# Kernel optimization log

Measured on AMD Instinct MI355X. Metric: run time of the kernel, lower is better.

The kernel has to match this reference:

```python
import jax, jax.numpy as jnp
import numpy as np

B, T, N, C, H, E = 1, 10, 10000, 4, 128, 160000


def setup_inputs() -> dict:
    key = jax.random.key(0)
    ks = jax.random.split(key, 16)
    def g(k, shape, fan_in):
        return jax.random.normal(k, shape, jnp.float32) / np.sqrt(fan_in).astype(np.float32)
    return {
        "inputs": jax.random.normal(ks[0], (B, T, N, C), jnp.float32),
        "msg_fc1_w": g(ks[1], (3, 2 * H, H), 2 * H),
        "msg_fc1_b": jnp.zeros((3, H), jnp.float32),
        "msg_fc2_w": g(ks[2], (3, H, H), H),
        "msg_fc2_b": jnp.zeros((3, H), jnp.float32),
        "hidden_r_w": g(ks[3], (H, H), H),
        "hidden_i_w": g(ks[4], (H, H), H),
        "hidden_h_w": g(ks[5], (H, H), H),
        "input_r_w": g(ks[6], (C, H), C),
        "input_r_b": jnp.zeros((H,), jnp.float32),
        "input_i_w": g(ks[7], (C, H), C),
        "input_i_b": jnp.zeros((H,), jnp.float32),
        "input_n_w": g(ks[8], (C, H), C),
        "input_n_b": jnp.zeros((H,), jnp.float32),
        "out1_w": g(ks[9], (H, H), H),
        "out1_b": jnp.zeros((H,), jnp.float32),
        "out2_w": g(ks[10], (H, H), H),
        "out2_b": jnp.zeros((H,), jnp.float32),
        "out3_w": g(ks[11], (H, C), H),
        "out3_b": jnp.zeros((C,), jnp.float32),
        "edge_index": jax.random.randint(ks[12], (2, E), 0, N, jnp.int32),
        "burn_in_steps": T,
    }


def reference(inputs, msg_fc1_w, msg_fc1_b, msg_fc2_w, msg_fc2_b,
              hidden_r_w, hidden_i_w, hidden_h_w,
              input_r_w, input_r_b, input_i_w, input_i_b, input_n_w, input_n_b,
              out1_w, out1_b, out2_w, out2_b, out3_w, out3_b,
              edge_index, burn_in_steps):
    row, col = edge_index[0], edge_index[1]
    Bv, Tv, Nv, Cv = inputs.shape
    Hv = hidden_r_w.shape[0]

    def single_step(x, hidden):
        # gather edge endpoint states: [B,E,2H]
        pre = jnp.concatenate([hidden[:, row, :], hidden[:, col, :]], axis=-1)
        # 3 msg branches vectorized over k (dropout p=0 / eval mode)
        m = jnp.tanh(jnp.einsum('bef,kfh->kbeh', pre, msg_fc1_w) + msg_fc1_b[:, None, None, :])
        m = jnp.tanh(jnp.einsum('kbeh,khd->kbed', m, msg_fc2_w) + msg_fc2_b[:, None, None, :])
        all_msgs = m.sum(0)  # [B,E,H]
        # scatter-add into receiver nodes (col)
        agg = jnp.zeros((Bv, Nv, Hv), x.dtype).at[:, col, :].add(all_msgs)
        r = jax.nn.sigmoid(x @ input_r_w + input_r_b + agg @ hidden_r_w)
        i = jax.nn.sigmoid(x @ input_i_w + input_i_b + agg @ hidden_i_w)
        n = jnp.tanh(x @ input_n_w + input_n_b + r * (agg @ hidden_h_w))
        hidden = (1 - i) * n + i * hidden
        p = jax.nn.relu(hidden @ out1_w + out1_b)
        p = jax.nn.relu(p @ out2_w + out2_b)
        p = jax.nn.relu(p @ out3_w + out3_b)
        return x + p, hidden

    def step(carry, xs):
        hidden, prev_pred = carry
        x_t, t = xs
        use_input = jnp.logical_or(t < burn_in_steps, t == 0)
        ins = jnp.where(use_input, x_t, prev_pred)
        pred, hidden = single_step(ins, hidden)
        return (hidden, pred), pred

    hidden0 = jnp.zeros((Bv, Nv, Hv), inputs.dtype)
    xs = (jnp.moveaxis(inputs, 1, 0), jnp.arange(Tv))  # [T,B,N,C]
    _, preds = jax.lax.scan(step, (hidden0, inputs[:, 0]), xs)
    return jnp.moveaxis(preds, 0, 1)  # [B,T,N,C]
```

## Files before the change

### kernel.cpp

```cpp
#include <hip/hip_runtime.h>

#define TT 10
#define NN 10000
#define CC 4
#define HH 128
#define EE 160000

typedef unsigned char u8;
typedef unsigned short u16;
typedef unsigned int u32;
typedef __attribute__((ext_vector_type(8))) short bf16x8;
typedef __attribute__((ext_vector_type(4))) float f32x4;

#define FW2 0
#define FW1 192
#define FO  768
#define FG  896
#define NFRAG 1184

__device__ __forceinline__ u16 f2b(float x){
  union { float f; u32 u; } v; v.f = x;
  return (u16)((v.u + 0x7fffu + ((v.u >> 16) & 1u)) >> 16);
}
__device__ __forceinline__ float b2f(u16 b){
  union { u32 u; float f; } v; v.u = ((u32)b) << 16;
  return v.f;
}
__device__ __forceinline__ float fast_tanh(float x){
  float e = __builtin_amdgcn_exp2f(x * 2.885390081777927f);
  return 1.f - 2.f * __builtin_amdgcn_rcpf(e + 1.f);
}
__device__ __forceinline__ f32x4 zero4(){ f32x4 z = {0.f,0.f,0.f,0.f}; return z; }
__device__ __forceinline__ f32x4 mfmab(bf16x8 a, bf16x8 b, f32x4 c){
  return __builtin_amdgcn_mfma_f32_16x16x32_bf16(a, b, c, 0, 0, 0);
}
__device__ __forceinline__ bf16x8 ldA(const u16* L, int row, int sl){
  return *(const bf16x8*)(L + (row << 7) + ((sl ^ (row & 7)) << 3));
}
__device__ __forceinline__ bf16x8 ldB(const u16* packs, int frag, int lane){
  return *(const bf16x8*)(packs + frag*512 + lane*8);
}

struct PSrc { const float* w2; const float* w1; const float* o1; const float* o2;
              const float* gr; const float* gi; const float* gh; };

__global__ void pack_weights(PSrc ps, u16* __restrict__ dst){
  int f = blockIdx.x, l = threadIdx.x;
  const float* src; int comp, kt, ct;
  if (f < 192){
    comp = f / 96; int g = f % 96;
    int br = g >> 5, rem = g & 31; kt = rem >> 3; ct = rem & 7;
    src = ps.w2 + (size_t)br*HH*HH;
  } else if (f < 768){
    int g = f - 192; int m = g / 96; int rem = g % 96;
    comp = rem >> 5; int idx = rem & 31; kt = idx >> 3; ct = idx & 7;
    src = ps.w1 + (size_t)m*HH*HH;
  } else if (f < 896){
    int g = f - 768; int mat = g >> 6; int rem = g & 63;
    comp = rem >> 5; int idx = rem & 31; kt = idx >> 3; ct = idx & 7;
    src = mat ? ps.o2 : ps.o1;
  } else {
    int g = f - 896; int mat = g / 96; int rem = g % 96;
    comp = rem >> 5; int idx = rem & 31; kt = idx >> 3; ct = idx & 7;
    src = mat == 0 ? ps.gr : (mat == 1 ? ps.gi : ps.gh);
  }
  int col = (ct << 4) + (l & 15);
  u16* d = dst + f*512 + l*8;
  #pragma unroll
  for (int j = 0; j < 8; ++j){
    int kk = (kt << 5) + ((l >> 4) << 3) + j;
    float v = src[kk*HH + col];
    u16 c0 = f2b(v); float r = v - b2f(c0);
    u16 c1 = f2b(r); r -= b2f(c1);
    u16 c2 = f2b(r);
    d[j] = comp == 0 ? c0 : (comp == 1 ? c1 : c2);
  }
}

__global__ void hist_kernel(const int* __restrict__ edge, int* __restrict__ hist){
  int i = blockIdx.x*256 + threadIdx.x;
  if (i < EE) atomicAdd(&hist[edge[EE + i]], 1);
}
__global__ void scan_kernel(const int* __restrict__ hist, int* __restrict__ cursor){
  __shared__ int part[256];
  __shared__ int partx[256];
  int tid = threadIdx.x;
  int base = tid*40;
  int s = 0;
  for (int j = 0; j < 40; ++j){ int b = base+j; if (b < NN) s += hist[b]; }
  part[tid] = s;
  __syncthreads();
  if (tid == 0){ int acc = 0; for (int i = 0; i < 256; ++i){ partx[i] = acc; acc += part[i]; } }
  __syncthreads();
  int acc = partx[tid];
  for (int j = 0; j < 40; ++j){ int b = base+j; if (b < NN){ cursor[b] = acc; acc += hist[b]; } }
}
__global__ void scatter_kernel(const int* __restrict__ edge, int* __restrict__ cursor,
                               int* __restrict__ pr, int* __restrict__ pc){
  int i = blockIdx.x*256 + threadIdx.x;
  if (i < EE){
    int r = edge[i], c = edge[EE + i];
    int pos = atomicAdd(&cursor[c], 1);
    pr[pos] = r; pc[pos] = c;
  }
}

__global__ __launch_bounds__(256)
void uv_kernel(const float* __restrict__ hid, const u16* __restrict__ packs,
               float* __restrict__ UV){
  __shared__ __align__(16) u16 h0[32*128], h1[32*128], h2[32*128];
  const int tid = threadIdx.x;
  const int lane = tid & 63, wid = tid >> 6;
  const int n0 = blockIdx.x << 5;

  #pragma unroll
  for (int it = 0; it < 4; ++it){
    int s = tid + (it << 8);
    int r = s >> 5, c4 = s & 31;
    int node = n0 + r; if (node > NN-1) node = NN-1;
    float4 v = *(const float4*)(hid + (size_t)node*HH + (c4 << 2));
    ushort4 q0, q1, q2;
    const float* pv = (const float*)&v;
    u16* q0p = (u16*)&q0; u16* q1p = (u16*)&q1; u16* q2p = (u16*)&q2;
    #pragma unroll
    for (int e = 0; e < 4; ++e){
      float x = pv[e];
      u16 a0 = f2b(x); float rr = x - b2f(a0);
      u16 a1 = f2b(rr); rr -= b2f(a1);
      q0p[e] = a0; q1p[e] = a1; q2p[e] = f2b(rr);
    }
    int idx = (r << 7) + (((c4 >> 1) ^ (r & 7)) << 3) + ((c4 & 1) << 2);
    *(ushort4*)(h0 + idx) = q0;
    *(ushort4*)(h1 + idx) = q1;
    *(ushort4*)(h2 + idx) = q2;
  }
  __syncthreads();

  const int ct0 = wid << 1;
  const int r0 = lane & 15, r1 = r0 + 16, kg = lane >> 4;

  for (int m = 0; m < 6; ++m){
    f32x4 acc[2][2];
    acc[0][0]=zero4(); acc[0][1]=zero4(); acc[1][0]=zero4(); acc[1][1]=zero4();
    #pragma unroll
    for (int kt = 0; kt < 4; ++kt){
      int sl = (kt << 2) + kg;
      bf16x8 a00 = ldA(h0, r0, sl), a01 = ldA(h1, r0, sl), a02 = ldA(h2, r0, sl);
      bf16x8 a10 = ldA(h0, r1, sl), a11 = ldA(h1, r1, sl), a12 = ldA(h2, r1, sl);
      #pragma unroll
      for (int ctl = 0; ctl < 2; ++ctl){
        int fb = FW1 + m*96 + (kt << 3) + ct0 + ctl;
        bf16x8 b0 = ldB(packs, fb,      lane);
        bf16x8 b1 = ldB(packs, fb + 32, lane);
        bf16x8 b2 = ldB(packs, fb + 64, lane);
        acc[0][ctl] = mfmab(a00, b0, acc[0][ctl]);
        acc[0][ctl] = mfmab(a01, b0, acc[0][ctl]);
        acc[0][ctl] = mfmab(a00, b1, acc[0][ctl]);
        acc[0][ctl] = mfmab(a02, b0, acc[0][ctl]);
        acc[0][ctl] = mfmab(a01, b1, acc[0][ctl]);
        acc[0][ctl] = mfmab(a00, b2, acc[0][ctl]);
        acc[1][ctl] = mfmab(a10, b0, acc[1][ctl]);
        acc[1][ctl] = mfmab(a11, b0, acc[1][ctl]);
        acc[1][ctl] = mfmab(a10, b1, acc[1][ctl]);
        acc[1][ctl] = mfmab(a12, b0, acc[1][ctl]);
        acc[1][ctl] = mfmab(a11, b1, acc[1][ctl]);
        acc[1][ctl] = mfmab(a10, b2, acc[1][ctl]);
      }
    }
    #pragma unroll
    for (int ctl = 0; ctl < 2; ++ctl)
      #pragma unroll
      for (int rt = 0; rt < 2; ++rt)
        #pragma unroll
        for (int j = 0; j < 4; ++j){
          int row = (rt << 4) + (kg << 2) + j;
          int col = ((ct0 + ctl) << 4) + r0;
          int node = n0 + row;
          if (node < NN) UV[((size_t)m*NN + node)*HH + col] = acc[rt][ctl][j];
        }
  }
}

__global__ __launch_bounds__(256)
void edge_kernel(const int* __restrict__ pr, const int* __restrict__ pc,
                 const float* __restrict__ UV,
                 const float* __restrict__ b1, const float* __restrict__ b2,
                 const u16* __restrict__ packs, float* __restrict__ agg){
  __shared__ __align__(16) u16 m1hi[32*128];
  __shared__ __align__(16) u16 m1lo[32*128];
  __shared__ int er[32], ec[32];
  const int tid = threadIdx.x;
  const int lane = tid & 63, wid = tid >> 6;
  const int e0 = blockIdx.x << 5;

  if (tid < 32) er[tid] = pr[e0 + tid];
  else if (tid < 64) ec[tid - 32] = pc[e0 + tid - 32];

  const int c4 = tid & 31;
  const int cOff = c4 << 2;
  const int ct0 = wid << 1;
  const int r0 = lane & 15, r1 = r0 + 16, kg = lane >> 4;

  f32x4 acc[2][2];
  acc[0][0]=zero4(); acc[0][1]=zero4(); acc[1][0]=zero4(); acc[1][1]=zero4();

  for (int k = 0; k < 3; ++k){
    __syncthreads();
    {
      float4 b = *(const float4*)(b1 + k*HH + cOff);
      const float* __restrict__ Ub = UV + (size_t)(2*k)*NN*HH;
      const float* __restrict__ Vb = UV + (size_t)(2*k + 1)*NN*HH;
      #pragma unroll
      for (int it = 0; it < 4; ++it){
        int e = (tid >> 5) + (it << 3);
        float4 u = *(const float4*)(Ub + (size_t)er[e]*HH + cOff);
        float4 v = *(const float4*)(Vb + (size_t)ec[e]*HH + cOff);
        float m0 = fast_tanh(u.x + v.x + b.x);
        float m1 = fast_tanh(u.y + v.y + b.y);
        float m2 = fast_tanh(u.z + v.z + b.z);
        float m3 = fast_tanh(u.w + v.w + b.w);
        ushort4 hi, lo;
        hi.x = f2b(m0); lo.x = f2b(m0 - b2f(hi.x));
        hi.y = f2b(m1); lo.y = f2b(m1 - b2f(hi.y));
        hi.z = f2b(m2); lo.z = f2b(m2 - b2f(hi.z));
        hi.w = f2b(m3); lo.w = f2b(m3 - b2f(hi.w));
        int idx = (e << 7) + (((c4 >> 1) ^ (e & 7)) << 3) + ((c4 & 1) << 2);
        *(ushort4*)(m1hi + idx) = hi;
        *(ushort4*)(m1lo + idx) = lo;
      }
    }
    __syncthreads();

    f32x4 lacc[2][2];
    lacc[0][0]=zero4(); lacc[0][1]=zero4(); lacc[1][0]=zero4(); lacc[1][1]=zero4();
    #pragma unroll
    for (int kt = 0; kt < 4; ++kt){
      int sl = (kt << 2) + kg;
      bf16x8 a0h = ldA(m1hi, r0, sl);
      bf16x8 a1h = ldA(m1hi, r1, sl);
      bf16x8 a0l = ldA(m1lo, r0, sl);
      bf16x8 a1l = ldA(m1lo, r1, sl);
      #pragma unroll
      for (int ctl = 0; ctl < 2; ++ctl){
        int fh = FW2 + k*32 + (kt << 3) + ct0 + ctl;
        bf16x8 bh = ldB(packs, fh, lane);
        bf16x8 bl = ldB(packs, fh + 96, lane);
        lacc[0][ctl] = mfmab(a0h, bh, lacc[0][ctl]);
        lacc[0][ctl] = mfmab(a0l, bh, lacc[0][ctl]);
        lacc[0][ctl] = mfmab(a0h, bl, lacc[0][ctl]);
        lacc[1][ctl] = mfmab(a1h, bh, lacc[1][ctl]);
        lacc[1][ctl] = mfmab(a1l, bh, lacc[1][ctl]);
        lacc[1][ctl] = mfmab(a1h, bl, lacc[1][ctl]);
      }
    }
    #pragma unroll
    for (int ctl = 0; ctl < 2; ++ctl){
      int col = ((ct0 + ctl) << 4) + r0;
      float bb = b2[k*HH + col];
      #pragma unroll
      for (int rt = 0; rt < 2; ++rt)
        #pragma unroll
        for (int j = 0; j < 4; ++j)
          acc[rt][ctl][j] += fast_tanh(lacc[rt][ctl][j] + bb);
    }
  }

  {
    int col0 = (ct0 << 4) + r0;
    int col1 = ((ct0 + 1) << 4) + r0;
    int prevNode = -1;
    float s0 = 0.f, s1 = 0.f;
    #pragma unroll
    for (int rt = 0; rt < 2; ++rt)
      #pragma unroll
      for (int j = 0; j < 4; ++j){
        int row = (rt << 4) + (kg << 2) + j;
        int node = ec[row];
        float v0 = acc[rt][0][j], v1 = acc[rt][1][j];
        if (node != prevNode){
          if (prevNode >= 0){
            atomicAdd(agg + (size_t)prevNode*HH + col0, s0);
            atomicAdd(agg + (size_t)prevNode*HH + col1, s1);
          }
          prevNode = node; s0 = v0; s1 = v1;
        } else { s0 += v0; s1 += v1; }
      }
    atomicAdd(agg + (size_t)prevNode*HH + col0, s0);
    atomicAdd(agg + (size_t)prevNode*HH + col1, s1);
  }
}

__global__ __launch_bounds__(256)
void node_kernel(const float* __restrict__ xin, const float* __restrict__ prevpred,
                 const int* __restrict__ burn, int t,
                 const float* __restrict__ agg, float* __restrict__ hid,
                 const float* __restrict__ irw, const float* __restrict__ irb,
                 const float* __restrict__ iiw, const float* __restrict__ iib,
                 const float* __restrict__ inw, const float* __restrict__ inb,
                 const float* __restrict__ o1b, const float* __restrict__ o2b,
                 const float* __restrict__ o3w, const float* __restrict__ o3b,
                 const u16* __restrict__ packs, float* __restrict__ out){
  __shared__ __align__(16) u16 ag0[32*128], ag1[32*128], ag2[32*128];
  __shared__ __align__(16) u16 hHi[32*128], hLo[32*128];
  __shared__ __align__(16) u16 p1Hi[32*128], p1Lo[32*128];
  __shared__ float p2L[32][136];
  __shared__ float xLs[32][4];
  const int tid = threadIdx.x;
  const int n0 = blockIdx.x << 5;
  const float* __restrict__ xs = (t == 0 || t < burn[0]) ? xin : prevpred;

  #pragma unroll
  for (int it = 0; it < 4; ++it){
    int s = tid + (it << 8);
    int r = s >> 5, c4 = s & 31;
    int node = n0 + r; if (node > NN-1) node = NN-1;
    float4 v = *(const float4*)(agg + (size_t)node*HH + (c4 << 2));
    ushort4 q0, q1, q2;
    const float* pv = (const float*)&v;
    u16* q0p = (u16*)&q0; u16* q1p = (u16*)&q1; u16* q2p = (u16*)&q2;
    #pragma unroll
    for (int e = 0; e < 4; ++e){
      float x = pv[e];
      u16 a0 = f2b(x); float rr = x - b2f(a0);
      u16 a1 = f2b(rr); rr -= b2f(a1);
      q0p[e] = a0; q1p[e] = a1; q2p[e] = f2b(rr);
    }
    int idx = (r << 7) + (((c4 >> 1) ^ (r & 7)) << 3) + ((c4 & 1) << 2);
    *(ushort4*)(ag0 + idx) = q0;
    *(ushort4*)(ag1 + idx) = q1;
    *(ushort4*)(ag2 + idx) = q2;
  }
  if (tid < 128){
    int r = tid >> 2, c = tid & 3;
    int node = n0 + r; if (node > NN-1) node = NN-1;
    xLs[r][c] = xs[(size_t)node*CC + c];
  }
  __syncthreads();

  const int lane = tid & 63, wid = tid >> 6;
  const int ct0 = wid << 1;
  const int r0 = lane & 15, r1 = r0 + 16, kg = lane >> 4;

  f32x4 aR[2][2], aI[2][2], aH[2][2];
  #pragma unroll
  for (int a = 0; a < 2; ++a){
    aR[a][0]=zero4(); aR[a][1]=zero4(); aI[a][0]=zero4(); aI[a][1]=zero4();
    aH[a][0]=zero4(); aH[a][1]=zero4();
  }
  #pragma unroll
  for (int kt = 0; kt < 4; ++kt){
    int sl = (kt << 2) + kg;
    bf16x8 a00 = ldA(ag0, r0, sl), a01 = ldA(ag1, r0, sl), a02 = ldA(ag2, r0, sl);
    bf16x8 a10 = ldA(ag0, r1, sl), a11 = ldA(ag1, r1, sl), a12 = ldA(ag2, r1, sl);
    #pragma unroll
    for (int ctl = 0; ctl < 2; ++ctl){
      #pragma unroll
      for (int m = 0; m < 3; ++m){
        int fb = FG + m*96 + (kt << 3) + ct0 + ctl;
        bf16x8 b0 = ldB(packs, fb,      lane);
        bf16x8 b1 = ldB(packs, fb + 32, lane);
        bf16x8 b2 = ldB(packs, fb + 64, lane);
        f32x4* A0 = m == 0 ? &aR[0][ctl] : (m == 1 ? &aI[0][ctl] : &aH[0][ctl]);
        f32x4* A1 = m == 0 ? &aR[1][ctl] : (m == 1 ? &aI[1][ctl] : &aH[1][ctl]);
        *A0 = mfmab(a00, b0, *A0);
        *A0 = mfmab(a01, b0, *A0);
        *A0 = mfmab(a00, b1, *A0);
        *A0 = mfmab(a02, b0, *A0);
        *A0 = mfmab(a01, b1, *A0);
        *A0 = mfmab(a00, b2, *A0);
        *A1 = mfmab(a10, b0, *A1);
        *A1 = mfmab(a11, b0, *A1);
        *A1 = mfmab(a10, b1, *A1);
        *A1 = mfmab(a12, b0, *A1);
        *A1 = mfmab(a11, b1, *A1);
        *A1 = mfmab(a10, b2, *A1);
      }
    }
  }

  #pragma unroll
  for (int ctl = 0; ctl < 2; ++ctl){
    int col = ((ct0 + ctl) << 4) + r0;
    float wr[CC], wi[CC], wn[CC];
    #pragma unroll
    for (int c = 0; c < CC; ++c){ wr[c]=irw[c*HH+col]; wi[c]=iiw[c*HH+col]; wn[c]=inw[c*HH+col]; }
    float rb = irb[col], ib = iib[col], nb = inb[col];
    #pragma unroll
    for (int rt = 0; rt < 2; ++rt)
      #pragma unroll
      for (int j = 0; j < 4; ++j){
        int row = (rt << 4) + (kg << 2) + j;
        int node = n0 + row;
        int nodec = node > NN-1 ? NN-1 : node;
        float xr = rb, xi = ib, xn = nb;
        #pragma unroll
        for (int c = 0; c < CC; ++c){
          float xv = xLs[row][c];
          xr = fmaf(xv, wr[c], xr); xi = fmaf(xv, wi[c], xi); xn = fmaf(xv, wn[c], xn);
        }
        float r = 1.f / (1.f + expf(-(xr + aR[rt][ctl][j])));
        float i = 1.f / (1.f + expf(-(xi + aI[rt][ctl][j])));
        float n = tanhf(xn + r * aH[rt][ctl][j]);
        float hold = hid[(size_t)nodec*HH + col];
        float hnew = (1.f - i)*n + i*hold;
        if (node < NN) hid[(size_t)node*HH + col] = hnew;
        u16 a = f2b(hnew);
        int idx = (row << 7) + (((col >> 3) ^ (row & 7)) << 3) + (col & 7);
        hHi[idx] = a;
        hLo[idx] = f2b(hnew - b2f(a));
      }
  }
  __syncthreads();

  {
    f32x4 q[2][2];
    q[0][0]=zero4(); q[0][1]=zero4(); q[1][0]=zero4(); q[1][1]=zero4();
    #pragma unroll
    for (int kt = 0; kt < 4; ++kt){
      int sl = (kt << 2) + kg;
      bf16x8 ah0 = ldA(hHi, r0, sl), al0 = ldA(hLo, r0, sl);
      bf16x8 ah1 = ldA(hHi, r1, sl), al1 = ldA(hLo, r1, sl);
      #pragma unroll
      for (int ctl = 0; ctl < 2; ++ctl){
        int fo = FO + (kt << 3) + ct0 + ctl;
        bf16x8 bh = ldB(packs, fo, lane);
        bf16x8 bl = ldB(packs, fo + 32, lane);
        q[0][ctl] = mfmab(ah0, bh, q[0][ctl]);
        q[0][ctl] = mfmab(al0, bh, q[0][ctl]);
        q[0][ctl] = mfmab(ah0, bl, q[0][ctl]);
        q[1][ctl] = mfmab(ah1, bh, q[1][ctl]);
        q[1][ctl] = mfmab(al1, bh, q[1][ctl]);
        q[1][ctl] = mfmab(ah1, bl, q[1][ctl]);
      }
    }
    #pragma unroll
    for (int ctl = 0; ctl < 2; ++ctl){
      int col = ((ct0 + ctl) << 4) + r0;
      float bb = o1b[col];
      #pragma unroll
      for (int rt = 0; rt < 2; ++rt)
        #pragma unroll
        for (int j = 0; j < 4; ++j){
          int row = (rt << 4) + (kg << 2) + j;
          float v = q[rt][ctl][j] + bb; v = v > 0.f ? v : 0.f;
          u16 a = f2b(v);
          int idx = (row << 7) + (((col >> 3) ^ (row & 7)) << 3) + (col & 7);
          p1Hi[idx] = a;
          p1Lo[idx] = f2b(v - b2f(a));
        }
    }
  }
  __syncthreads();

  {
    f32x4 q[2][2];
    q[0][0]=zero4(); q[0][1]=zero4(); q[1][0]=zero4(); q[1][1]=zero4();
    #pragma unroll
    for (int kt = 0; kt < 4; ++kt){
      int sl = (kt << 2) + kg;
      bf16x8 ah0 = ldA(p1Hi, r0, sl), al0 = ldA(p1Lo, r0, sl);
      bf16x8 ah1 = ldA(p1Hi, r1, sl), al1 = ldA(p1Lo, r1, sl);
      #pragma unroll
      for (int ctl = 0; ctl < 2; ++ctl){
        int fo = FO + 64 + (kt << 3) + ct0 + ctl;
        bf16x8 bh = ldB(packs, fo, lane);
        bf16x8 bl = ldB(packs, fo + 32, lane);
        q[0][ctl] = mfmab(ah0, bh, q[0][ctl]);
        q[0][ctl] = mfmab(al0, bh, q[0][ctl]);
        q[0][ctl] = mfmab(ah0, bl, q[0][ctl]);
        q[1][ctl] = mfmab(ah1, bh, q[1][ctl]);
        q[1][ctl] = mfmab(al1, bh, q[1][ctl]);
        q[1][ctl] = mfmab(ah1, bl, q[1][ctl]);
      }
    }
    #pragma unroll
    for (int ctl = 0; ctl < 2; ++ctl){
      int col = ((ct0 + ctl) << 4) + r0;
      float bb = o2b[col];
      #pragma unroll
      for (int rt = 0; rt < 2; ++rt)
        #pragma unroll
        for (int j = 0; j < 4; ++j){
          int row = (rt << 4) + (kg << 2) + j;
          float v = q[rt][ctl][j] + bb; v = v > 0.f ? v : 0.f;
          p2L[row][col] = v;
        }
    }
  }
  __syncthreads();

  if (tid < 128){
    int r = tid >> 2, c = tid & 3;
    int node = n0 + r;
    if (node < NN){
      float s = o3b[c];
      for (int kk = 0; kk < HH; ++kk) s = fmaf(p2L[r][kk], o3w[kk*CC + c], s);
      float v = fmaxf(s, 0.f);
      out[((size_t)t*NN + node)*CC + c] = xLs[r][c] + v;
    }
  }
}

extern "C" void kernel_launch(void* const* d_in, const int* in_sizes, int n_in,
                              void* d_out, int out_size, void* d_ws, size_t ws_size,
                              hipStream_t stream){
  const float* inputs = (const float*)d_in[0];
  const float* fc1w = (const float*)d_in[1];
  const float* fc1b = (const float*)d_in[2];
  const float* fc2w = (const float*)d_in[3];
  const float* fc2b = (const float*)d_in[4];
  const float* whr  = (const float*)d_in[5];
  const float* whi  = (const float*)d_in[6];
  const float* whh  = (const float*)d_in[7];
  const float* irw  = (const float*)d_in[8];
  const float* irb  = (const float*)d_in[9];
  const float* iiw  = (const float*)d_in[10];
  const float* iib  = (const float*)d_in[11];
  const float* inw  = (const float*)d_in[12];
  const float* inb  = (const float*)d_in[13];
  const float* o1w  = (const float*)d_in[14];
  const float* o1b  = (const float*)d_in[15];
  const float* o2w  = (const float*)d_in[16];
  const float* o2b  = (const float*)d_in[17];
  const float* o3w  = (const float*)d_in[18];
  const float* o3b  = (const float*)d_in[19];
  const int* edge   = (const int*)d_in[20];
  const int* burn   = (const int*)d_in[21];
  float* out = (float*)d_out;

  u8* ws = (u8*)d_ws;
  float* hid   = (float*)(ws);
  float* agg   = (float*)(ws + 5120000);
  float* UV    = (float*)(ws + 10240000);
  u16*   packs = (u16*)(ws + 40960000);
  int*   pr    = (int*)(ws + 42172416);
  int*   pc    = (int*)(ws + 42812416);
  int*   hist  = (int*)(ws + 43452416);
  int*   cursor= (int*)(ws + 43492416);

  hipMemsetAsync(hid, 0, 5120000, stream);
  hipMemsetAsync(hist, 0, 40000, stream);

  PSrc ps; ps.w2 = fc2w; ps.w1 = fc1w; ps.o1 = o1w; ps.o2 = o2w;
  ps.gr = whr; ps.gi = whi; ps.gh = whh;
  hipLaunchKernelGGL(pack_weights, dim3(NFRAG), dim3(64), 0, stream, ps, packs);
  hipLaunchKernelGGL(hist_kernel, dim3((EE+255)/256), dim3(256), 0, stream, edge, hist);
  hipLaunchKernelGGL(scan_kernel, dim3(1), dim3(256), 0, stream, hist, cursor);
  hipLaunchKernelGGL(scatter_kernel, dim3((EE+255)/256), dim3(256), 0, stream, edge, cursor, pr, pc);

  const int nblk = (NN + 31) / 32;
  for (int t = 0; t < TT; ++t){
    hipMemsetAsync(agg, 0, 5120000, stream);
    hipLaunchKernelGGL(uv_kernel, dim3(nblk), dim3(256), 0, stream, hid, packs, UV);
    hipLaunchKernelGGL(edge_kernel, dim3(EE/32), dim3(256), 0, stream,
                       pr, pc, UV, fc1b, fc2b, packs, agg);
    hipLaunchKernelGGL(node_kernel, dim3(nblk), dim3(256), 0, stream,
                       inputs + (size_t)t*NN*CC, out + (size_t)(t > 0 ? t-1 : 0)*NN*CC, burn, t,
                       agg, hid, irw, irb, iiw, iib, inw, inb,
                       o1b, o2b, o3w, o3b, packs, out);
  }
}
```

Baseline: 1.728 ms.

## Fuse UV projection into node kernel and double-buffer edge message staging

Removes the separate uv_kernel. The node kernel now splits the new hidden state into three bf16 terms in shared memory, reusing the aggregate buffers, and computes the next step's U/V projections right away, so hidden is not re-read from global memory and one launch per step goes away. Initial UV is zeroed by a memset, which matches the zero initial hidden state. The edge kernel double-buffers its message tile, staging branch k+1 while branch k runs its MFMA. This costs more shared memory and registers in both kernels, which may lower occupancy.

```diff
diff --git a/kernel.cpp b/kernel.cpp
--- a/kernel.cpp
+++ b/kernel.cpp
@@ -106,88 +106,12 @@
 }
 
 __global__ __launch_bounds__(256)
-void uv_kernel(const float* __restrict__ hid, const u16* __restrict__ packs,
-               float* __restrict__ UV){
-  __shared__ __align__(16) u16 h0[32*128], h1[32*128], h2[32*128];
-  const int tid = threadIdx.x;
-  const int lane = tid & 63, wid = tid >> 6;
-  const int n0 = blockIdx.x << 5;
-
-  #pragma unroll
-  for (int it = 0; it < 4; ++it){
-    int s = tid + (it << 8);
-    int r = s >> 5, c4 = s & 31;
-    int node = n0 + r; if (node > NN-1) node = NN-1;
-    float4 v = *(const float4*)(hid + (size_t)node*HH + (c4 << 2));
-    ushort4 q0, q1, q2;
-    const float* pv = (const float*)&v;
-    u16* q0p = (u16*)&q0; u16* q1p = (u16*)&q1; u16* q2p = (u16*)&q2;
-    #pragma unroll
-    for (int e = 0; e < 4; ++e){
-      float x = pv[e];
-      u16 a0 = f2b(x); float rr = x - b2f(a0);
-      u16 a1 = f2b(rr); rr -= b2f(a1);
-      q0p[e] = a0; q1p[e] = a1; q2p[e] = f2b(rr);
-    }
-    int idx = (r << 7) + (((c4 >> 1) ^ (r & 7)) << 3) + ((c4 & 1) << 2);
-    *(ushort4*)(h0 + idx) = q0;
-    *(ushort4*)(h1 + idx) = q1;
-    *(ushort4*)(h2 + idx) = q2;
-  }
-  __syncthreads();
-
-  const int ct0 = wid << 1;
-  const int r0 = lane & 15, r1 = r0 + 16, kg = lane >> 4;
-
-  for (int m = 0; m < 6; ++m){
-    f32x4 acc[2][2];
-    acc[0][0]=zero4(); acc[0][1]=zero4(); acc[1][0]=zero4(); acc[1][1]=zero4();
-    #pragma unroll
-    for (int kt = 0; kt < 4; ++kt){
-      int sl = (kt << 2) + kg;
-      bf16x8 a00 = ldA(h0, r0, sl), a01 = ldA(h1, r0, sl), a02 = ldA(h2, r0, sl);
-      bf16x8 a10 = ldA(h0, r1, sl), a11 = ldA(h1, r1, sl), a12 = ldA(h2, r1, sl);
-      #pragma unroll
-      for (int ctl = 0; ctl < 2; ++ctl){
-        int fb = FW1 + m*96 + (kt << 3) + ct0 + ctl;
-        bf16x8 b0 = ldB(packs, fb,      lane);
-        bf16x8 b1 = ldB(packs, fb + 32, lane);
-        bf16x8 b2 = ldB(packs, fb + 64, lane);
-        acc[0][ctl] = mfmab(a00, b0, acc[0][ctl]);
-        acc[0][ctl] = mfmab(a01, b0, acc[0][ctl]);
-        acc[0][ctl] = mfmab(a00, b1, acc[0][ctl]);
-        acc[0][ctl] = mfmab(a02, b0, acc[0][ctl]);
-        acc[0][ctl] = mfmab(a01, b1, acc[0][ctl]);
-        acc[0][ctl] = mfmab(a00, b2, acc[0][ctl]);
-        acc[1][ctl] = mfmab(a10, b0, acc[1][ctl]);
-        acc[1][ctl] = mfmab(a11, b0, acc[1][ctl]);
-        acc[1][ctl] = mfmab(a10, b1, acc[1][ctl]);
-        acc[1][ctl] = mfmab(a12, b0, acc[1][ctl]);
-        acc[1][ctl] = mfmab(a11, b1, acc[1][ctl]);
-        acc[1][ctl] = mfmab(a10, b2, acc[1][ctl]);
-      }
-    }
-    #pragma unroll
-    for (int ctl = 0; ctl < 2; ++ctl)
-      #pragma unroll
-      for (int rt = 0; rt < 2; ++rt)
-        #pragma unroll
-        for (int j = 0; j < 4; ++j){
-          int row = (rt << 4) + (kg << 2) + j;
-          int col = ((ct0 + ctl) << 4) + r0;
-          int node = n0 + row;
-          if (node < NN) UV[((size_t)m*NN + node)*HH + col] = acc[rt][ctl][j];
-        }
-  }
-}
-
-__global__ __launch_bounds__(256)
 void edge_kernel(const int* __restrict__ pr, const int* __restrict__ pc,
                  const float* __restrict__ UV,
                  const float* __restrict__ b1, const float* __restrict__ b2,
                  const u16* __restrict__ packs, float* __restrict__ agg){
-  __shared__ __align__(16) u16 m1hi[32*128];
-  __shared__ __align__(16) u16 m1lo[32*128];
+  __shared__ __align__(16) u16 m1hi[2][32*128];
+  __shared__ __align__(16) u16 m1lo[2][32*128];
   __shared__ int er[32], ec[32];
   const int tid = threadIdx.x;
   const int lane = tid & 63, wid = tid >> 6;
@@ -195,51 +119,60 @@
 
   if (tid < 32) er[tid] = pr[e0 + tid];
   else if (tid < 64) ec[tid - 32] = pc[e0 + tid - 32];
+  __syncthreads();
 
   const int c4 = tid & 31;
   const int cOff = c4 << 2;
   const int ct0 = wid << 1;
   const int r0 = lane & 15, r1 = r0 + 16, kg = lane >> 4;
 
+  auto stage = [&](int k, int b){
+    float4 bb = *(const float4*)(b1 + k*HH + cOff);
+    const float* __restrict__ Ub = UV + (size_t)(2*k)*NN*HH;
+    const float* __restrict__ Vb = UV + (size_t)(2*k + 1)*NN*HH;
+    u16* hiB = &m1hi[b][0];
+    u16* loB = &m1lo[b][0];
+    #pragma unroll
+    for (int it = 0; it < 4; ++it){
+      int e = (tid >> 5) + (it << 3);
+      float4 u = *(const float4*)(Ub + (size_t)er[e]*HH + cOff);
+      float4 v = *(const float4*)(Vb + (size_t)ec[e]*HH + cOff);
+      float m0 = fast_tanh(u.x + v.x + bb.x);
+      float m1 = fast_tanh(u.y + v.y + bb.y);
+      float m2 = fast_tanh(u.z + v.z + bb.z);
+      float m3 = fast_tanh(u.w + v.w + bb.w);
+      ushort4 hi, lo;
+      hi.x = f2b(m0); lo.x = f2b(m0 - b2f(hi.x));
+      hi.y = f2b(m1); lo.y = f2b(m1 - b2f(hi.y));
+      hi.z = f2b(m2); lo.z = f2b(m2 - b2f(hi.z));
+      hi.w = f2b(m3); lo.w = f2b(m3 - b2f(hi.w));
+      int idx = (e << 7) + (((c4 >> 1) ^ (e & 7)) << 3) + ((c4 & 1) << 2);
+      *(ushort4*)(hiB + idx) = hi;
+      *(ushort4*)(loB + idx) = lo;
+    }
+  };
+
   f32x4 acc[2][2];
   acc[0][0]=zero4(); acc[0][1]=zero4(); acc[1][0]=zero4(); acc[1][1]=zero4();
 
+  stage(0, 0);
+  __syncthreads();
+
   for (int k = 0; k < 3; ++k){
-    __syncthreads();
-    {
-      float4 b = *(const float4*)(b1 + k*HH + cOff);
-      const float* __restrict__ Ub = UV + (size_t)(2*k)*NN*HH;
-      const float* __restrict__ Vb = UV + (size_t)(2*k + 1)*NN*HH;
-      #pragma unroll
-      for (int it = 0; it < 4; ++it){
-        int e = (tid >> 5) + (it << 3);
-        float4 u = *(const float4*)(Ub + (size_t)er[e]*HH + cOff);
-        float4 v = *(const float4*)(Vb + (size_t)ec[e]*HH + cOff);
-        float m0 = fast_tanh(u.x + v.x + b.x);
-        float m1 = fast_tanh(u.y + v.y + b.y);
-        float m2 = fast_tanh(u.z + v.z + b.z);
-        float m3 = fast_tanh(u.w + v.w + b.w);
-        ushort4 hi, lo;
-        hi.x = f2b(m0); lo.x = f2b(m0 - b2f(hi.x));
-        hi.y = f2b(m1); lo.y = f2b(m1 - b2f(hi.y));
-        hi.z = f2b(m2); lo.z = f2b(m2 - b2f(hi.z));
-        hi.w = f2b(m3); lo.w = f2b(m3 - b2f(hi.w));
-        int idx = (e << 7) + (((c4 >> 1) ^ (e & 7)) << 3) + ((c4 & 1) << 2);
-        *(ushort4*)(m1hi + idx) = hi;
-        *(ushort4*)(m1lo + idx) = lo;
-      }
-    }
-    __syncthreads();
-
+    int cur = k & 1;
+    if (k < 2) stage(k + 1, cur ^ 1);
+
+    const u16* hiB = &m1hi[cur][0];
+    const u16* loB = &m1lo[cur][0];
     f32x4 lacc[2][2];
     lacc[0][0]=zero4(); lacc[0][1]=zero4(); lacc[1][0]=zero4(); lacc[1][1]=zero4();
     #pragma unroll
     for (int kt = 0; kt < 4; ++kt){
       int sl = (kt << 2) + kg;
-      bf16x8 a0h = ldA(m1hi, r0, sl);
-      bf16x8 a1h = ldA(m1hi, r1, sl);
-      bf16x8 a0l = ldA(m1lo, r0, sl);
-      bf16x8 a1l = ldA(m1lo, r1, sl);
+      bf16x8 a0h = ldA(hiB, r0, sl);
+      bf16x8 a1h = ldA(hiB, r1, sl);
+      bf16x8 a0l = ldA(loB, r0, sl);
+      bf16x8 a1l = ldA(loB, r1, sl);
       #pragma unroll
       for (int ctl = 0; ctl < 2; ++ctl){
         int fh = FW2 + k*32 + (kt << 3) + ct0 + ctl;
@@ -263,6 +196,7 @@
         for (int j = 0; j < 4; ++j)
           acc[rt][ctl][j] += fast_tanh(lacc[rt][ctl][j] + bb);
     }
+    __syncthreads();
   }
 
   {
@@ -299,9 +233,9 @@
                  const float* __restrict__ inw, const float* __restrict__ inb,
                  const float* __restrict__ o1b, const float* __restrict__ o2b,
                  const float* __restrict__ o3w, const float* __restrict__ o3b,
-                 const u16* __restrict__ packs, float* __restrict__ out){
+                 const u16* __restrict__ packs, float* __restrict__ UV,
+                 float* __restrict__ out){
   __shared__ __align__(16) u16 ag0[32*128], ag1[32*128], ag2[32*128];
-  __shared__ __align__(16) u16 hHi[32*128], hLo[32*128];
   __shared__ __align__(16) u16 p1Hi[32*128], p1Lo[32*128];
   __shared__ float p2L[32][136];
   __shared__ float xLs[32][4];
@@ -377,6 +311,7 @@
       }
     }
   }
+  __syncthreads();
 
   #pragma unroll
   for (int ctl = 0; ctl < 2; ++ctl){
@@ -404,10 +339,12 @@
         float hold = hid[(size_t)nodec*HH + col];
         float hnew = (1.f - i)*n + i*hold;
         if (node < NN) hid[(size_t)node*HH + col] = hnew;
-        u16 a = f2b(hnew);
+        u16 a = f2b(hnew); float rr = hnew - b2f(a);
+        u16 b = f2b(rr);   rr -= b2f(b);
         int idx = (row << 7) + (((col >> 3) ^ (row & 7)) << 3) + (col & 7);
-        hHi[idx] = a;
-        hLo[idx] = f2b(hnew - b2f(a));
+        ag0[idx] = a;
+        ag1[idx] = b;
+        ag2[idx] = f2b(rr);
       }
   }
   __syncthreads();
@@ -418,8 +355,8 @@
     #pragma unroll
     for (int kt = 0; kt < 4; ++kt){
       int sl = (kt << 2) + kg;
-      bf16x8 ah0 = ldA(hHi, r0, sl), al0 = ldA(hLo, r0, sl);
-      bf16x8 ah1 = ldA(hHi, r1, sl), al1 = ldA(hLo, r1, sl);
+      bf16x8 ah0 = ldA(ag0, r0, sl), al0 = ldA(ag1, r0, sl);
+      bf16x8 ah1 = ldA(ag0, r1, sl), al1 = ldA(ag1, r1, sl);
       #pragma unroll
       for (int ctl = 0; ctl < 2; ++ctl){
         int fo = FO + (kt << 3) + ct0 + ctl;
@@ -488,6 +425,49 @@
     }
   }
   __syncthreads();
+
+  if (t < TT-1){
+    for (int m = 0; m < 6; ++m){
+      f32x4 acc[2][2];
+      acc[0][0]=zero4(); acc[0][1]=zero4(); acc[1][0]=zero4(); acc[1][1]=zero4();
+      #pragma unroll
+      for (int kt = 0; kt < 4; ++kt){
+        int sl = (kt << 2) + kg;
+        bf16x8 a00 = ldA(ag0, r0, sl), a01 = ldA(ag1, r0, sl), a02 = ldA(ag2, r0, sl);
+        bf16x8 a10 = ldA(ag0, r1, sl), a11 = ldA(ag1, r1, sl), a12 = ldA(ag2, r1, sl);
+        #pragma unroll
+        for (int ctl = 0; ctl < 2; ++ctl){
+          int fb = FW1 + m*96 + (kt << 3) + ct0 + ctl;
+          bf16x8 b0 = ldB(packs, fb,      lane);
+          bf16x8 b1 = ldB(packs, fb + 32, lane);
+          bf16x8 b2 = ldB(packs, fb + 64, lane);
+          acc[0][ctl] = mfmab(a00, b0, acc[0][ctl]);
+          acc[0][ctl] = mfmab(a01, b0, acc[0][ctl]);
+          acc[0][ctl] = mfmab(a00, b1, acc[0][ctl]);
+          acc[0][ctl] = mfmab(a02, b0, acc[0][ctl]);
+          acc[0][ctl] = mfmab(a01, b1, acc[0][ctl]);
+          acc[0][ctl] = mfmab(a00, b2, acc[0][ctl]);
+          acc[1][ctl] = mfmab(a10, b0, acc[1][ctl]);
+          acc[1][ctl] = mfmab(a11, b0, acc[1][ctl]);
+          acc[1][ctl] = mfmab(a10, b1, acc[1][ctl]);
+          acc[1][ctl] = mfmab(a12, b0, acc[1][ctl]);
+          acc[1][ctl] = mfmab(a11, b1, acc[1][ctl]);
+          acc[1][ctl] = mfmab(a10, b2, acc[1][ctl]);
+        }
+      }
+      #pragma unroll
+      for (int ctl = 0; ctl < 2; ++ctl)
+        #pragma unroll
+        for (int rt = 0; rt < 2; ++rt)
+          #pragma unroll
+          for (int j = 0; j < 4; ++j){
+            int row = (rt << 4) + (kg << 2) + j;
+            int col = ((ct0 + ctl) << 4) + r0;
+            int node = n0 + row;
+            if (node < NN) UV[((size_t)m*NN + node)*HH + col] = acc[rt][ctl][j];
+          }
+    }
+  }
 
   if (tid < 128){
     int r = tid >> 2, c = tid & 3;
@@ -539,6 +519,7 @@
   int*   cursor= (int*)(ws + 43492416);
 
   hipMemsetAsync(hid, 0, 5120000, stream);
+  hipMemsetAsync(UV, 0, 30720000, stream);
   hipMemsetAsync(hist, 0, 40000, stream);
 
   PSrc ps; ps.w2 = fc2w; ps.w1 = fc1w; ps.o1 = o1w; ps.o2 = o2w;
@@ -551,12 +532,11 @@
   const int nblk = (NN + 31) / 32;
   for (int t = 0; t < TT; ++t){
     hipMemsetAsync(agg, 0, 5120000, stream);
-    hipLaunchKernelGGL(uv_kernel, dim3(nblk), dim3(256), 0, stream, hid, packs, UV);
     hipLaunchKernelGGL(edge_kernel, dim3(EE/32), dim3(256), 0, stream,
                        pr, pc, UV, fc1b, fc2b, packs, agg);
     hipLaunchKernelGGL(node_kernel, dim3(nblk), dim3(256), 0, stream,
                        inputs + (size_t)t*NN*CC, out + (size_t)(t > 0 ? t-1 : 0)*NN*CC, burn, t,
                        agg, hid, irw, irb, iiw, iib, inw, inb,
-                       o1b, o2b, o3w, o3b, packs, out);
-  }
-}
+                       o1b, o2b, o3w, o3b, packs, UV, out);
+  }
+}
```

Result: faster. 1.568 ms (-9.3%).
